# Performance work log

Hardware: AMD Instinct MI355X
Metric: run time of the kernel (lower is better)

Reference implementation:

```python
import jax, jax.numpy as jnp
import numpy as np

D_SVG, N_TYPE, N_PAR = 256, 10, 12          # deep-svg latent, animation types, animation params
PADDING_VALUE = -1.0
W_SVG, W_TYPE, W_PAR = 10.0, 0.1, 1.0       # weight_deep_svg, weight_type, weight_parameters

# ANIMATION_PARAMETER_INDICES as a dense boolean lookup: type t -> which params it uses
_pm = np.zeros((N_TYPE, N_PAR), dtype=bool)
for _t in range(N_TYPE):
    for _k in (_t % N_PAR, (_t + 1) % N_PAR, (_t + 2) % N_PAR):
        _pm[_t, _k] = True
PARAM_MASK = jnp.asarray(_pm)


def setup_inputs() -> dict:
    B, S = 256, 512
    F = D_SVG + N_TYPE + N_PAR
    key = jax.random.key(0)
    k1, k2, k3, k4, k5 = jax.random.split(key, 5)
    x = jax.random.normal(k1, (B, S, F), dtype=jnp.float32)
    cls = jax.random.randint(k2, (B, S), 0, N_TYPE)
    t_type = jax.nn.one_hot(cls, N_TYPE, dtype=jnp.float32)
    t_svg = jax.random.normal(k3, (B, S, D_SVG), dtype=jnp.float32)
    t_par = jax.random.normal(k4, (B, S, N_PAR), dtype=jnp.float32)
    target = jnp.concatenate([t_svg, t_type, t_par], axis=-1)
    # suffix-contiguous padding (matches the `break` semantics of the torch loop)
    lengths = jax.random.randint(k5, (B,), S // 2, S + 1)
    mask = jnp.arange(S)[None, :] >= lengths[:, None]            # True = padded
    target = jnp.where(mask[..., None], PADDING_VALUE, target)
    return {"input": x, "target": target, "target_padding_mask": mask}


def reference(input, target, target_padding_mask):
    # input[expanded_mask] = -100
    x = jnp.where(target_padding_mask[..., None], -100.0, input)
    in_svg, in_type, in_par = jnp.split(x, [D_SVG, D_SVG + N_TYPE], axis=-1)
    tg_svg, tg_type, tg_par = jnp.split(target, [D_SVG, D_SVG + N_TYPE], axis=-1)

    valid = tg_type[..., 0] != PADDING_VALUE                      # [B,S] non-padded rows
    t_idx = jnp.argmax(tg_type, axis=-1)                          # [B,S] animation type

    # vectorized replacement of the double for-loop: copy target params at the
    # type-dependent ANIMATION_PARAMETER_INDICES into input params
    pmask = PARAM_MASK[t_idx] & valid[..., None]                  # [B,S,N_PAR]
    in_par = jnp.where(pmask, tg_par, in_par)

    # CrossEntropyLoss(ignore_index=-1) over flattened type logits
    logits = in_type.reshape(-1, N_TYPE)
    labels = t_idx.reshape(-1)
    v = valid.reshape(-1).astype(logits.dtype)
    logp = jax.nn.log_softmax(logits, axis=-1)
    nll = -jnp.take_along_axis(logp, labels[:, None], axis=1)[:, 0]
    loss_type = jnp.sum(nll * v) / jnp.maximum(jnp.sum(v), 1.0)

    # plain MSE (mean over ALL elements, padding included, as in the original)
    loss_svg = jnp.mean((in_svg - tg_svg) ** 2)
    loss_par = jnp.mean((in_par - tg_par) ** 2)

    return W_SVG * loss_svg + W_TYPE * loss_type + W_PAR * loss_par
```

## Files before the change

kernel.cpp:

```cpp
#include <hip/hip_runtime.h>
#include <math.h>

#define D_SVG 256
#define N_TYPE 10
#define N_PAR 12
#define F_TOT (D_SVG + N_TYPE + N_PAR)
#define ROWS_PER_BLOCK 32
#define THREADS 256
#define N4_PER_BLOCK (ROWS_PER_BLOCK * F_TOT / 4)
#define N4_ITERS ((N4_PER_BLOCK + THREADS - 1) / THREADS)


__global__ __launch_bounds__(THREADS) void fused_kernel(const float* __restrict__ input,
                                                        const float* __restrict__ target,
                                                        float4* __restrict__ part,
                                                        unsigned* __restrict__ bitmap) {
    __shared__ float sred[4][4];
    const int tid  = threadIdx.x;
    const int lane = tid & 63, wave = tid >> 6;
    const long row0 = (long)blockIdx.x * ROWS_PER_BLOCK;

    bool vld = false;
    if (lane < 32) vld = (target[(row0 + lane) * F_TOT + D_SVG] != -1.0f);
    const unsigned bits = (unsigned)__ballot(vld);

    if (bits == 0u) {
        if (tid == 0) { part[blockIdx.x] = make_float4(0.f, 0.f, 0.f, 0.f);
                        bitmap[blockIdx.x] = 0u; }
        return;
    }

    float nll = 0.0f, corr = 0.0f;
    if (tid < 32 && ((bits >> tid) & 1u)) {
        const long rb = (row0 + tid) * F_TOT;
        const float2* __restrict__ tg2 = (const float2*)(target + rb + D_SVG);
        const float2* __restrict__ in2 = (const float2*)(input  + rb + D_SVG);
        float tt[N_TYPE], l[N_TYPE];
        #pragma unroll
        for (int j = 0; j < 5; ++j) { float2 v = tg2[j]; tt[2*j] = v.x; tt[2*j+1] = v.y; }
        #pragma unroll
        for (int j = 0; j < 5; ++j) { float2 v = in2[j]; l[2*j]  = v.x; l[2*j+1]  = v.y; }
        int ti = 0; float best = tt[0];
        #pragma unroll
        for (int j = 1; j < N_TYPE; ++j) { if (tt[j] > best) { best = tt[j]; ti = j; } }
        float m = l[0];
        #pragma unroll
        for (int j = 1; j < N_TYPE; ++j) m = fmaxf(m, l[j]);
        float s = 0.0f;
        #pragma unroll
        for (int j = 0; j < N_TYPE; ++j) s += __expf(l[j] - m);
        nll = __logf(s) + m - l[ti];
        const long p = rb + (D_SVG + N_TYPE) + ti;
        float d0 = input[p]     - target[p];
        float d1 = input[p + 1] - target[p + 1];
        float d2 = input[p + 2] - target[p + 2];
        corr = d0 * d0 + d1 * d1 + d2 * d2;
    }

    const unsigned k   = (unsigned)__popc(bits);
    const unsigned pre = (k == 32u) ? 0xffffffffu : ((1u << k) - 1u);
    const unsigned n4v = (bits == pre) ? ((k * (unsigned)F_TOT + 3u) >> 2)
                                       : (unsigned)N4_PER_BLOCK;

    const float4* __restrict__ in4p = (const float4*)(input  + row0 * F_TOT);
    const float4* __restrict__ tg4p = (const float4*)(target + row0 * F_TOT);

    float svg = 0.0f, par = 0.0f;

    auto accum = [&](unsigned idx, float4 ivv, float4 tvv) {
        unsigned e0 = idx * 4u;
        unsigned ra = e0 / (unsigned)F_TOT;
        unsigned rb = (e0 + 2u) / (unsigned)F_TOT;
        unsigned fa = e0 - ra * (unsigned)F_TOT;
        unsigned fb = (e0 + 2u) - rb * (unsigned)F_TOT;
        unsigned vA = (bits >> ra) & 1u;
        unsigned vB = (bits >> rb) & 1u;
        float xs[4] = {ivv.x, ivv.y, ivv.z, ivv.w};
        float ts[4] = {tvv.x, tvv.y, tvv.z, tvv.w};
        #pragma unroll
        for (int j = 0; j < 4; ++j) {
            unsigned v    = (j < 2) ? vA : vB;
            unsigned feat = ((j < 2) ? fa : fb) + (unsigned)(j & 1);
            float d = xs[j] - ts[j];
            float sq = d * d;
            svg += (v && feat < D_SVG) ? sq : 0.0f;
            par += (v && feat >= D_SVG + N_TYPE) ? sq : 0.0f;
        }
    };

    float4 iv[N4_ITERS], tv[N4_ITERS];
    #pragma unroll
    for (int u = 0; u < N4_ITERS; ++u) {
        unsigned idx = (unsigned)tid + u * THREADS;
        if (idx < n4v) { iv[u] = in4p[idx]; tv[u] = tg4p[idx]; }
    }
    #pragma unroll
    for (int u = 0; u < N4_ITERS; ++u) {
        unsigned idx = (unsigned)tid + u * THREADS;
        if (idx < n4v) accum(idx, iv[u], tv[u]);
    }

    float vals[4] = {svg, par, nll, corr};
    #pragma unroll
    for (int v = 0; v < 4; ++v) {
        float x = vals[v];
        #pragma unroll
        for (int off = 32; off > 0; off >>= 1) x += __shfl_down(x, off, 64);
        vals[v] = x;
    }
    if (lane == 0) {
        #pragma unroll
        for (int v = 0; v < 4; ++v) sred[wave][v] = vals[v];
    }
    __syncthreads();
    if (tid == 0) {
        float s0 = sred[0][0] + sred[1][0] + sred[2][0] + sred[3][0];
        float s1 = sred[0][1] + sred[1][1] + sred[2][1] + sred[3][1];
        float s2 = sred[0][2] + sred[1][2] + sred[2][2] + sred[3][2];
        float s3 = sred[0][3] + sred[1][3] + sred[2][3] + sred[3][3];
        part[blockIdx.x]   = make_float4(s0, s1, s2, s3);
        bitmap[blockIdx.x] = bits;
    }
}

__global__ __launch_bounds__(256) void loss_final(const float4* __restrict__ part,
                                                  const unsigned* __restrict__ bitmap,
                                                  float* __restrict__ out,
                                                  int nb, int nrows) {
    __shared__ double sred[4][5];
    const int tid = threadIdx.x;
    double svg = 0.0, par = 0.0, nll = 0.0, corr = 0.0, cnt = 0.0;
    for (int i = tid; i < nb; i += 256) {
        float4 v = part[i];
        svg += v.x; par += v.y; nll += v.z; corr += v.w;
        cnt += (double)__popc(bitmap[i]);
    }
    double vals[5] = {svg, par, nll, corr, cnt};
    #pragma unroll
    for (int v = 0; v < 5; ++v) {
        double x = vals[v];
        #pragma unroll
        for (int off = 32; off > 0; off >>= 1) x += __shfl_down(x, off, 64);
        vals[v] = x;
    }
    const int wave = tid >> 6, lane = tid & 63;
    if (lane == 0) {
        #pragma unroll
        for (int v = 0; v < 5; ++v) sred[wave][v] = vals[v];
    }
    __syncthreads();
    if (tid == 0) {
        double S[5];
        #pragma unroll
        for (int v = 0; v < 5; ++v)
            S[v] = sred[0][v] + sred[1][v] + sred[2][v] + sred[3][v];
        double npad = (double)nrows - S[4];
        double svg_t = S[0] + 9801.0 * D_SVG * npad;
        double par_t = S[1] - S[3] + 9801.0 * N_PAR * npad;
        double loss = 10.0 * svg_t / ((double)nrows * D_SVG)
                    + 0.1  * S[2] / fmax(S[4], 1.0)
                    + 1.0  * par_t / ((double)nrows * N_PAR);
        out[0] = (float)loss;
    }
}

extern "C" void kernel_launch(void* const* d_in, const int* in_sizes, int n_in,
                              void* d_out, int out_size, void* d_ws, size_t ws_size,
                              hipStream_t stream) {
    const float* input  = (const float*)d_in[0];
    const float* target = (const float*)d_in[1];
    float* out = (float*)d_out;

    const int nrows = in_sizes[0] / F_TOT;
    const int blk   = nrows / ROWS_PER_BLOCK;

    float4*   part   = (float4*)d_ws;
    unsigned* bitmap = (unsigned*)((char*)d_ws + (size_t)blk * sizeof(float4));

    fused_kernel<<<blk, THREADS, 0, stream>>>(input, target, part, bitmap);
    loss_final<<<1, 256, 0, stream>>>(part, bitmap, out, blk, nrows);
}
```

Baseline: 290.9 us.

## Precompute validity bitmap in separate kernel and stage type/param sections via LDS

Moves the per-row padding check into a separate bitmap kernel so the main kernel no longer has a dependent load and ballot before its bulk streaming loads. The type-logit and parameter sections are captured into shared memory during the main float4 pass, and the cross-entropy and correction terms are computed from LDS after a barrier rather than re-read from global memory. The cost is an extra kernel launch with a strided read of one target element per row, plus scattered LDS writes and an added barrier.

Result: no change. 294.0 us (+1.1%).

```diff
diff --git a/kernel.cpp b/kernel.cpp
--- a/kernel.cpp
+++ b/kernel.cpp
@@ -9,53 +9,38 @@
 #define THREADS 256
 #define N4_PER_BLOCK (ROWS_PER_BLOCK * F_TOT / 4)
 #define N4_ITERS ((N4_PER_BLOCK + THREADS - 1) / THREADS)
+#define SEC (N_TYPE + N_PAR)
 
+
+__global__ __launch_bounds__(256) void bitmap_kernel(const float* __restrict__ target,
+                                                     unsigned* __restrict__ bitmap) {
+    const int tid = threadIdx.x;
+    const long r = (long)blockIdx.x * 256 + tid;
+    const bool valid = (target[r * F_TOT + D_SVG] != -1.0f);
+    unsigned long long bal = __ballot(valid);
+    const int lane = tid & 63, wv = tid >> 6;
+    if (lane == 0)  bitmap[blockIdx.x * 8 + wv * 2]     = (unsigned)bal;
+    if (lane == 32) bitmap[blockIdx.x * 8 + wv * 2 + 1] = (unsigned)(bal >> 32);
+}
 
 __global__ __launch_bounds__(THREADS) void fused_kernel(const float* __restrict__ input,
                                                         const float* __restrict__ target,
-                                                        float4* __restrict__ part,
-                                                        unsigned* __restrict__ bitmap) {
+                                                        const unsigned* __restrict__ bitmap,
+                                                        float4* __restrict__ part) {
+    __shared__ float s_in[ROWS_PER_BLOCK][SEC];
+    __shared__ float s_tg[ROWS_PER_BLOCK][SEC];
     __shared__ float sred[4][4];
     const int tid  = threadIdx.x;
     const int lane = tid & 63, wave = tid >> 6;
-    const long row0 = (long)blockIdx.x * ROWS_PER_BLOCK;
 
-    bool vld = false;
-    if (lane < 32) vld = (target[(row0 + lane) * F_TOT + D_SVG] != -1.0f);
-    const unsigned bits = (unsigned)__ballot(vld);
+    const unsigned bits = bitmap[blockIdx.x];
 
     if (bits == 0u) {
-        if (tid == 0) { part[blockIdx.x] = make_float4(0.f, 0.f, 0.f, 0.f);
-                        bitmap[blockIdx.x] = 0u; }
+        if (tid == 0) part[blockIdx.x] = make_float4(0.f, 0.f, 0.f, 0.f);
         return;
     }
 
-    float nll = 0.0f, corr = 0.0f;
-    if (tid < 32 && ((bits >> tid) & 1u)) {
-        const long rb = (row0 + tid) * F_TOT;
-        const float2* __restrict__ tg2 = (const float2*)(target + rb + D_SVG);
-        const float2* __restrict__ in2 = (const float2*)(input  + rb + D_SVG);
-        float tt[N_TYPE], l[N_TYPE];
-        #pragma unroll
-        for (int j = 0; j < 5; ++j) { float2 v = tg2[j]; tt[2*j] = v.x; tt[2*j+1] = v.y; }
-        #pragma unroll
-        for (int j = 0; j < 5; ++j) { float2 v = in2[j]; l[2*j]  = v.x; l[2*j+1]  = v.y; }
-        int ti = 0; float best = tt[0];
-        #pragma unroll
-        for (int j = 1; j < N_TYPE; ++j) { if (tt[j] > best) { best = tt[j]; ti = j; } }
-        float m = l[0];
-        #pragma unroll
-        for (int j = 1; j < N_TYPE; ++j) m = fmaxf(m, l[j]);
-        float s = 0.0f;
-        #pragma unroll
-        for (int j = 0; j < N_TYPE; ++j) s += __expf(l[j] - m);
-        nll = __logf(s) + m - l[ti];
-        const long p = rb + (D_SVG + N_TYPE) + ti;
-        float d0 = input[p]     - target[p];
-        float d1 = input[p + 1] - target[p + 1];
-        float d2 = input[p + 2] - target[p + 2];
-        corr = d0 * d0 + d1 * d1 + d2 * d2;
-    }
+    const long row0 = (long)blockIdx.x * ROWS_PER_BLOCK;
 
     const unsigned k   = (unsigned)__popc(bits);
     const unsigned pre = (k == 32u) ? 0xffffffffu : ((1u << k) - 1u);
@@ -79,12 +64,17 @@
         float ts[4] = {tvv.x, tvv.y, tvv.z, tvv.w};
         #pragma unroll
         for (int j = 0; j < 4; ++j) {
+            unsigned row  = (j < 2) ? ra : rb;
+            unsigned feat = ((j < 2) ? fa : fb) + (unsigned)(j & 1);
             unsigned v    = (j < 2) ? vA : vB;
-            unsigned feat = ((j < 2) ? fa : fb) + (unsigned)(j & 1);
             float d = xs[j] - ts[j];
             float sq = d * d;
             svg += (v && feat < D_SVG) ? sq : 0.0f;
             par += (v && feat >= D_SVG + N_TYPE) ? sq : 0.0f;
+            if (feat >= D_SVG) {
+                s_in[row][feat - D_SVG] = xs[j];
+                s_tg[row][feat - D_SVG] = ts[j];
+            }
         }
     };
 
@@ -98,6 +88,30 @@
     for (int u = 0; u < N4_ITERS; ++u) {
         unsigned idx = (unsigned)tid + u * THREADS;
         if (idx < n4v) accum(idx, iv[u], tv[u]);
+    }
+
+    __syncthreads();
+
+    float nll = 0.0f, corr = 0.0f;
+    if (tid < 32 && ((bits >> tid) & 1u)) {
+        float tt[N_TYPE], l[N_TYPE];
+        #pragma unroll
+        for (int j = 0; j < N_TYPE; ++j) { tt[j] = s_tg[tid][j]; l[j] = s_in[tid][j]; }
+        int ti = 0; float best = tt[0];
+        #pragma unroll
+        for (int j = 1; j < N_TYPE; ++j) { if (tt[j] > best) { best = tt[j]; ti = j; } }
+        float m = l[0];
+        #pragma unroll
+        for (int j = 1; j < N_TYPE; ++j) m = fmaxf(m, l[j]);
+        float s = 0.0f;
+        #pragma unroll
+        for (int j = 0; j < N_TYPE; ++j) s += __expf(l[j] - m);
+        nll = __logf(s) + m - l[ti];
+        #pragma unroll
+        for (int j = 0; j < 3; ++j) {
+            float d = s_in[tid][N_TYPE + ti + j] - s_tg[tid][N_TYPE + ti + j];
+            corr += d * d;
+        }
     }
 
     float vals[4] = {svg, par, nll, corr};
@@ -118,8 +132,7 @@
         float s1 = sred[0][1] + sred[1][1] + sred[2][1] + sred[3][1];
         float s2 = sred[0][2] + sred[1][2] + sred[2][2] + sred[3][2];
         float s3 = sred[0][3] + sred[1][3] + sred[2][3] + sred[3][3];
-        part[blockIdx.x]   = make_float4(s0, s1, s2, s3);
-        bitmap[blockIdx.x] = bits;
+        part[blockIdx.x] = make_float4(s0, s1, s2, s3);
     }
 }
 
@@ -173,10 +186,12 @@
 
     const int nrows = in_sizes[0] / F_TOT;
     const int blk   = nrows / ROWS_PER_BLOCK;
+    const int blk_m = nrows / 256;
 
     float4*   part   = (float4*)d_ws;
     unsigned* bitmap = (unsigned*)((char*)d_ws + (size_t)blk * sizeof(float4));
 
-    fused_kernel<<<blk, THREADS, 0, stream>>>(input, target, part, bitmap);
+    bitmap_kernel<<<blk_m, 256, 0, stream>>>(target, bitmap);
+    fused_kernel<<<blk, THREADS, 0, stream>>>(input, target, bitmap, part);
     loss_final<<<1, 256, 0, stream>>>(part, bitmap, out, blk, nrows);
 }
```
